# Kernel optimization log

Measured on AMD Instinct MI355X. Metric: run time of the kernel, lower is better.

Reference implementation:

```python
import jax, jax.numpy as jnp
import numpy as np

B, L, D, H = 4, 2048, 256, 8
FF = 128  # ff_intermediary_depth hard-coded in module
EPS = 1e-5


def layer_norm(x, g, b):
    mu = jnp.mean(x, axis=-1, keepdims=True)
    var = jnp.mean(jnp.square(x - mu), axis=-1, keepdims=True)
    return (x - mu) * jax.lax.rsqrt(var + EPS) * g + b


def setup_inputs() -> dict:
    key = jax.random.key(0)
    ks = jax.random.split(key, 8)
    s = 1.0 / np.sqrt(D)
    return {
        "seq": jax.random.normal(ks[0], (B, L, D), dtype=jnp.float32),
        "Wq": jax.random.normal(ks[1], (D, D * H), dtype=jnp.float32) * s,
        "Wk": jax.random.normal(ks[2], (D, D * H), dtype=jnp.float32) * s,
        "Wv": jax.random.normal(ks[3], (D, D * H), dtype=jnp.float32) * s,
        "Wo": jax.random.normal(ks[4], (D * H, D), dtype=jnp.float32) * (1.0 / np.sqrt(D * H)),
        "ln1_g": jnp.ones((D,), jnp.float32),
        "ln1_b": jnp.zeros((D,), jnp.float32),
        "W1": jax.random.normal(ks[5], (D, FF), dtype=jnp.float32) * s,
        "b1": jnp.zeros((FF,), jnp.float32),
        "W2": jax.random.normal(ks[6], (FF, D), dtype=jnp.float32) * (1.0 / np.sqrt(FF)),
        "b2": jnp.zeros((D,), jnp.float32),
        "ln2_g": jnp.ones((D,), jnp.float32),
        "ln2_b": jnp.zeros((D,), jnp.float32),
    }


def reference(seq, Wq, Wk, Wv, Wo, ln1_g, ln1_b, W1, b1, W2, b2, ln2_g, ln2_b):
    b, l, d = seq.shape
    # per-head dim equals full depth d (module quirk)
    q = (seq @ Wq).reshape(b, l, H, d)
    k = (seq @ Wk).reshape(b, l, H, d)
    v = (seq @ Wv).reshape(b, l, H, d)
    scores = jnp.einsum('bqhd,bkhd->bhqk', q, k) / jnp.sqrt(jnp.float32(d))
    a = jax.nn.softmax(scores, axis=-1)
    heads = jnp.einsum('bhqk,bkhd->bqhd', a, v).reshape(b, l, H * d)
    att_out = heads @ Wo
    x = layer_norm(seq + att_out, ln1_g, ln1_b)
    ff = jax.nn.relu(x @ W1 + b1) @ W2 + b2
    return layer_norm(x + ff, ln2_g, ln2_b)
```

## Files before the change

kernel.cpp:

```cpp
#include <hip/hip_runtime.h>


typedef unsigned short u16;
typedef unsigned int   u32;
typedef __bf16 bf16x8 __attribute__((ext_vector_type(8)));
typedef __bf16 bf16x2 __attribute__((ext_vector_type(2)));
typedef float  f32x4  __attribute__((ext_vector_type(4)));

#define MFMA(a, b, c) __builtin_amdgcn_mfma_f32_16x16x32_bf16(a, b, c, 0, 0, 0)

#if __has_builtin(__builtin_amdgcn_exp2f)
#define EXP2(x) __builtin_amdgcn_exp2f(x)
#else
#define EXP2(x) exp2f(x)
#endif

#if __has_builtin(__builtin_amdgcn_permlane16_swap) && \
    __has_builtin(__builtin_amdgcn_permlane32_swap)
#define HAS_PERMSWAP 1
#else
#define HAS_PERMSWAP 0
#endif

#define CEXP 0.09016844f

__device__ __forceinline__ float b2f(u16 h) {
  return __uint_as_float(((u32)h) << 16);
}
__device__ __forceinline__ u16 f2b(float f) {
  u32 u = __float_as_uint(f);
  u += 0x7FFFu + ((u >> 16) & 1u);
  return (u16)(u >> 16);
}
__device__ __forceinline__ u32 pkbf(float lo, float hi) {
  bf16x2 v;
  v[0] = (__bf16)lo;
  v[1] = (__bf16)hi;
  return __builtin_bit_cast(u32, v);
}
__device__ __forceinline__ bf16x8 ldb8(const u16* p) { return *(const bf16x8*)p; }

typedef const __attribute__((address_space(1))) u32* gas1_t;
typedef __attribute__((address_space(3))) u32* las3_t;
__device__ __forceinline__ void gload_lds16(const u16* g, u16* lds_base) {
  __builtin_amdgcn_global_load_lds((gas1_t)(const void*)g,
                                   (las3_t)(void*)lds_base, 16, 0, 0);
}

__device__ __forceinline__ int detect_f32(const void* seq) {
  const u32* s = (const u32*)seq;
  int cnt = 0;
  #pragma unroll
  for (int i = 0; i < 64; i++) {
    u32 e = (s[i] >> 7) & 0xFFu;
    cnt += (e >= 100u && e <= 140u) ? 1 : 0;
  }
  return cnt < 48;
}

__device__ __forceinline__ u16 ldw(const void* W, size_t idx, int isf32) {
  return isf32 ? f2b(((const float*)W)[idx]) : ((const u16*)W)[idx];
}

#if HAS_PERMSWAP
__device__ __forceinline__ bf16x8 softmax_pa(f32x4 sn0, f32x4 sn1,
                                             float& lsum) {
  float p00 = EXP2(sn0[0]), p01 = EXP2(sn0[1]);
  float p02 = EXP2(sn0[2]), p03 = EXP2(sn0[3]);
  float p10 = EXP2(sn1[0]), p11 = EXP2(sn1[1]);
  float p12 = EXP2(sn1[2]), p13 = EXP2(sn1[3]);
  lsum += ((p00 + p01) + (p02 + p03)) + ((p10 + p11) + (p12 + p13));
  u32 A0 = pkbf(p00, p01), A1 = pkbf(p02, p03);
  u32 B0 = pkbf(p10, p11), B1 = pkbf(p12, p13);
  auto ra = __builtin_amdgcn_permlane32_swap(A0, B0, false, false);
  auto rb = __builtin_amdgcn_permlane32_swap(A1, B1, false, false);
  auto sa = __builtin_amdgcn_permlane16_swap(ra[0], ra[1], false, false);
  auto sb = __builtin_amdgcn_permlane16_swap(rb[0], rb[1], false, false);
  uint4 wv;
  wv.x = sa[0];
  wv.y = sb[0];
  wv.z = sa[1];
  wv.w = sb[1];
  return __builtin_bit_cast(bf16x8, wv);
}
#endif

__global__ __launch_bounds__(256) void ingest_kernel(
    const void* __restrict__ seq, const void* __restrict__ g1,
    const void* __restrict__ be1, const void* __restrict__ b1,
    const void* __restrict__ b2v, const void* __restrict__ g2,
    const void* __restrict__ be2, u16* __restrict__ sbuf,
    u16* __restrict__ vecs) {
  int isf32 = detect_f32(seq);
  int bx = blockIdx.x, tid = threadIdx.x;
  if (bx < 2048) {
    size_t i = (size_t)bx * 1024 + tid * 4;
    if (isf32) {
      const float* sp = (const float*)seq;
      u16 o0 = f2b(sp[i]), o1 = f2b(sp[i + 1]), o2 = f2b(sp[i + 2]), o3 = f2b(sp[i + 3]);
      uint2 ov; ov.x = (u32)o0 | ((u32)o1 << 16); ov.y = (u32)o2 | ((u32)o3 << 16);
      *(uint2*)(sbuf + i) = ov;
    } else {
      *(uint2*)(sbuf + i) = ((const uint2*)seq)[i >> 2];
    }
  } else {
    int t = bx - 2048;
    const void* src; int n;
    switch (t) {
      case 0: src = g1;  n = 256; break;
      case 1: src = be1; n = 256; break;
      case 2: src = b1;  n = 128; break;
      case 3: src = b2v; n = 256; break;
      case 4: src = g2;  n = 256; break;
      default: src = be2; n = 256; break;
    }
    if (tid < n) vecs[t * 256 + tid] = ldw(src, tid, isf32);
  }
}

__global__ __launch_bounds__(256) void pack_kernel(
    const void* __restrict__ Wq, const void* __restrict__ Wk,
    const void* __restrict__ Wv, const void* __restrict__ Wo,
    const void* __restrict__ W1, const void* __restrict__ W2,
    const void* __restrict__ seq,
    u16* __restrict__ pWq, u16* __restrict__ pWk, u16* __restrict__ pWv,
    u16* __restrict__ pWo, u16* __restrict__ pW1, u16* __restrict__ pW2) {
  int isf32 = detect_f32(seq);
  const void* W; u16* P; int K, N;
  switch (blockIdx.y) {
    case 0: W = Wq; P = pWq; K = 256;  N = 2048; break;
    case 1: W = Wk; P = pWk; K = 256;  N = 2048; break;
    case 2: W = Wv; P = pWv; K = 256;  N = 2048; break;
    case 3: W = Wo; P = pWo; K = 2048; N = 256;  break;
    case 4: W = W1; P = pW1; K = 256;  N = 128;  break;
    default: W = W2; P = pW2; K = 128; N = 256;  break;
  }
  int t = blockIdx.x * 256 + threadIdx.x;
  int total = (K >> 5) * (N >> 4) * 64;
  if (t >= total) return;
  int lane = t & 63, f = t >> 6;
  int NT = N >> 4;
  int kt = f / NT, nt = f - kt * NT;
  int row0 = kt * 32 + ((lane >> 4) << 3);
  int col = nt * 16 + (lane & 15);
  u16 e[8];
  #pragma unroll
  for (int j = 0; j < 8; j++) e[j] = ldw(W, (size_t)(row0 + j) * N + col, isf32);
  uint4 u;
  u.x = (u32)e[0] | ((u32)e[1] << 16);
  u.y = (u32)e[2] | ((u32)e[3] << 16);
  u.z = (u32)e[4] | ((u32)e[5] << 16);
  u.w = (u32)e[6] | ((u32)e[7] << 16);
  *(uint4*)(P + ((size_t)f * 64 + lane) * 8) = u;
}

__global__ __launch_bounds__(256, 2) void qkv_kernel(
    const u16* __restrict__ X,
    const u16* __restrict__ pWq, const u16* __restrict__ pWk,
    const u16* __restrict__ pWv,
    u16* __restrict__ Qo, u16* __restrict__ Ko, u16* __restrict__ Vo,
    int ntbase, int hc) {
  __shared__ u16 blds[64 * 512];
  const u16* Pw = (blockIdx.z == 0) ? pWq : ((blockIdx.z == 1) ? pWk : pWv);
  u16* Out = (blockIdx.z == 0) ? Qo : ((blockIdx.z == 1) ? Ko : Vo);
  int tid = threadIdx.x, lane = tid & 63, w = tid >> 6;
  int nt0 = ntbase + blockIdx.x * 8;
  int m0 = blockIdx.y * 128 + w * 32;
  bf16x8 af[2][8];
  #pragma unroll
  for (int kt = 0; kt < 8; kt++) {
    af[0][kt] = ldb8(X + (size_t)(m0 + (lane & 15)) * 256 + kt * 32 + (lane >> 4) * 8);
    af[1][kt] = ldb8(X + (size_t)(m0 + 16 + (lane & 15)) * 256 + kt * 32 + (lane >> 4) * 8);
  }
  #pragma unroll
  for (int i = 0; i < 16; i++) {
    int fl = w + i * 4;
    int kt = fl >> 3, nt = fl & 7;
    gload_lds16(Pw + ((size_t)(kt * 128 + nt0 + nt) * 64 + lane) * 8,
                blds + (size_t)fl * 512);
  }
  asm volatile("s_waitcnt vmcnt(0)" ::: "memory");
  __syncthreads();
  f32x4 acc[2][8] = {};
  #pragma unroll
  for (int kt = 0; kt < 8; kt++) {
    const u16* bp = blds + (size_t)kt * 8 * 512 + (size_t)lane * 8;
    #pragma unroll
    for (int nt = 0; nt < 8; nt++) {
      bf16x8 b = ldb8(bp + nt * 512);
      acc[0][nt] = MFMA(af[0][kt], b, acc[0][nt]);
      acc[1][nt] = MFMA(af[1][kt], b, acc[1][nt]);
    }
  }
  int isv = (blockIdx.z == 2);
  float sc = (blockIdx.z == 0) ? CEXP : 1.0f;
  int hl = blockIdx.x >> 1;
  int dd0 = (blockIdx.x & 1) * 128;
  int m0b = blockIdx.y * 128;
  int bi = m0b >> 11, l0 = m0b & 2047;
  __syncthreads();
  if (!isv) {
    #pragma unroll
    for (int mt = 0; mt < 2; mt++)
      #pragma unroll
      for (int nt = 0; nt < 8; nt++)
        #pragma unroll
        for (int r = 0; r < 4; r++)
          blds[(w * 32 + mt * 16 + (lane >> 4) * 4 + r) * 136 + nt * 16 + (lane & 15)] =
              f2b(acc[mt][nt][r] * sc);
    __syncthreads();
    #pragma unroll
    for (int i = 0; i < 8; i++) {
      int c = tid + i * 256;
      int mloc = c >> 4, q = c & 15;
      uint4 v = *(uint4*)(blds + mloc * 136 + q * 8);
      *(uint4*)(Out + ((size_t)(bi * hc + hl) * 2048 + l0 + mloc) * 256 + dd0 + q * 8) = v;
    }
  } else {
    #pragma unroll
    for (int mt = 0; mt < 2; mt++)
      #pragma unroll
      for (int nt = 0; nt < 8; nt++)
        #pragma unroll
        for (int r = 0; r < 4; r++)
          blds[(nt * 16 + (lane & 15)) * 136 + w * 32 + mt * 16 + (lane >> 4) * 4 + r] =
              f2b(acc[mt][nt][r]);
    __syncthreads();
    #pragma unroll
    for (int i = 0; i < 8; i++) {
      int c = tid + i * 256;
      int nloc = c >> 4, q = c & 15;
      uint4 v = *(uint4*)(blds + nloc * 136 + q * 8);
      *(uint4*)(Out + ((size_t)(bi * hc + hl) * 256 + dd0 + nloc) * 2048 + l0 + q * 8) = v;
    }
  }
}

__global__ __launch_bounds__(512, 4) void attn_kernel(
    const u16* __restrict__ Q, const u16* __restrict__ K,
    const u16* __restrict__ Vt, u16* __restrict__ O, int nbh) {
  __shared__ u16 kbuf[2 * 8192];
  __shared__ u16 vbuf[2 * 8192];
#if !HAS_PERMSWAP
  __shared__ u16 plds[8 * 640];
#endif
  int tid = threadIdx.x, lane = tid & 63, w = tid >> 6;
  int bi2 = blockIdx.x;
  int bh, qt;
  if (nbh >= 8) {
    int G = nbh >> 3;
    bh = (bi2 & 7) * G + (bi2 >> 3) % G;
    qt = bi2 / (8 * G);
  } else {
    bh = bi2 % nbh; qt = bi2 / nbh;
  }
  const u16* Qb  = Q  + (size_t)bh * 2048 * 256;
  const u16* Kb  = K  + (size_t)bh * 2048 * 256;
  const u16* Vtb = Vt + (size_t)bh * 256 * 2048;
  u16* Ob = O + (size_t)bh * 2048 * 256;
  int q0 = qt * 128 + w * 16;
  bf16x8 qf[8];
  #pragma unroll
  for (int kt = 0; kt < 8; kt++)
    qf[kt] = ldb8(Qb + (size_t)(q0 + (lane & 15)) * 256 + kt * 32 + (lane >> 4) * 8);
  f32x4 o[16] = {};
  float lsum = 0.f;
#if !HAS_PERMSWAP
  u16* pl = plds + (size_t)w * 640;
#endif

  #pragma unroll
  for (int j = 0; j < 2; j++) {
    int f = w * 2 + j;
    gload_lds16(Kb + (size_t)((f >> 3) * 16 + (lane & 15)) * 256 +
                    (f & 7) * 32 + (lane >> 4) * 8,
                kbuf + f * 512);
    gload_lds16(Vtb + (size_t)(f * 16 + (lane & 15)) * 2048 + (lane >> 4) * 8,
                vbuf + f * 512);
  }

  for (int t = 0; t < 64; t++) {
    int s0i = t * 32;
    asm volatile("s_waitcnt vmcnt(0)\ns_barrier" ::: "memory");
    if (t < 63) {
      int nb = (t + 1) & 1;
      #pragma unroll
      for (int j = 0; j < 2; j++) {
        int f = w * 2 + j;
        gload_lds16(Kb + (size_t)(s0i + 32 + (f >> 3) * 16 + (lane & 15)) * 256 +
                        (f & 7) * 32 + (lane >> 4) * 8,
                    kbuf + nb * 8192 + f * 512);
        gload_lds16(Vtb + (size_t)(f * 16 + (lane & 15)) * 2048 + s0i + 32 +
                        (lane >> 4) * 8,
                    vbuf + nb * 8192 + f * 512);
      }
    }
    const u16* kb = kbuf + (t & 1) * 8192;
    f32x4 s[2] = {};
    __builtin_amdgcn_s_setprio(1);
    #pragma unroll
    for (int ntk = 0; ntk < 2; ntk++)
      #pragma unroll
      for (int kt = 0; kt < 8; kt++) {
        bf16x8 a = ldb8(kb + (size_t)(ntk * 8 + kt) * 512 + lane * 8);
        s[ntk] = MFMA(a, qf[kt], s[ntk]);
      }
    __builtin_amdgcn_s_setprio(0);
#if HAS_PERMSWAP
    bf16x8 pa = softmax_pa(s[0], s[1], lsum);
#else
    #pragma unroll
    for (int ntk = 0; ntk < 2; ntk++) {
      float p0 = EXP2(s[ntk][0]);
      float p1 = EXP2(s[ntk][1]);
      float p2 = EXP2(s[ntk][2]);
      float p3 = EXP2(s[ntk][3]);
      lsum += (p0 + p1) + (p2 + p3);
      uint2 pk;
      pk.x = pkbf(p0, p1);
      pk.y = pkbf(p2, p3);
      *(uint2*)(pl + (lane & 15) * 40 + 16 * ntk + 4 * (lane >> 4)) = pk;
    }
    asm volatile("s_waitcnt lgkmcnt(0)" ::: "memory");
    bf16x8 pa = ldb8(pl + (lane & 15) * 40 + (lane >> 4) * 8);
    asm volatile("s_waitcnt lgkmcnt(0)" ::: "memory");
#endif
    const u16* vb0 = vbuf + (t & 1) * 8192;
    __builtin_amdgcn_s_setprio(1);
    #pragma unroll
    for (int nt = 0; nt < 16; nt++) {
      bf16x8 vb = ldb8(vb0 + (size_t)nt * 512 + lane * 8);
      o[nt] = MFMA(vb, pa, o[nt]);
    }
    __builtin_amdgcn_s_setprio(0);
  }
  float l = lsum;
  l += __shfl_xor(l, 16);
  l += __shfl_xor(l, 32);
  float linv = 1.0f / l;
  u16* el = kbuf + w * 1152;
  __syncthreads();
  #pragma unroll
  for (int g = 0; g < 4; g++) {
    if (g) asm volatile("s_waitcnt lgkmcnt(0)" ::: "memory");
    #pragma unroll
    for (int t2 = 0; t2 < 4; t2++) {
      int nt = g * 4 + t2;
      uint2 pk;
      pk.x = pkbf(o[nt][0] * linv, o[nt][1] * linv);
      pk.y = pkbf(o[nt][2] * linv, o[nt][3] * linv);
      *(uint2*)(el + (lane & 15) * 72 + t2 * 16 + 4 * (lane >> 4)) = pk;
    }
    asm volatile("s_waitcnt lgkmcnt(0)" ::: "memory");
    #pragma unroll
    for (int rep = 0; rep < 2; rep++) {
      int ch = lane + rep * 64;
      int row = ch >> 3, c8 = ch & 7;
      uint4 v = *(uint4*)(el + row * 72 + c8 * 8);
      *(uint4*)(Ob + (size_t)(q0 + row) * 256 + g * 64 + c8 * 8) = v;
    }
  }
}

__global__ __launch_bounds__(128) void accum_ln1_kernel(
    const u16* __restrict__ Oc, const u16* __restrict__ pWo,
    const u16* __restrict__ sbuf, const u16* __restrict__ vecs,
    u16* __restrict__ xout) {
  __shared__ u16 blds[2 * 32 * 512];
  int tid = threadIdx.x, lane = tid & 63, w = tid >> 6;
  int m0 = blockIdx.x * 32 + w * 16;
  int arow = m0 + (lane & 15);
  int bq = arow >> 11, lrow = arow & 2047;
  f32x4 acc[16] = {};
  #pragma unroll
  for (int i = 0; i < 16; i++) {
    int fl = w + i * 2;
    int ktg = fl >> 4, nt = fl & 15;
    gload_lds16(pWo + ((size_t)(ktg * 16 + nt) * 64 + lane) * 8,
                blds + (size_t)fl * 512);
  }
  asm volatile("s_waitcnt vmcnt(0)" ::: "memory");
  __syncthreads();
  for (int r = 0; r < 32; r++) {
    int k0 = r * 2;
    const u16* cur = blds + (size_t)(r & 1) * 16384;
    bf16x8 aA, aB;
    {
      int ktl = k0, hl = ktl >> 3;
      int d0 = (ktl & 7) * 32 + (lane >> 4) * 8;
      aA = ldb8(Oc + ((size_t)(bq * 8 + hl) * 2048 + lrow) * 256 + d0);
      ktl = k0 + 1; hl = ktl >> 3;
      d0 = (ktl & 7) * 32 + (lane >> 4) * 8;
      aB = ldb8(Oc + ((size_t)(bq * 8 + hl) * 2048 + lrow) * 256 + d0);
    }
    if (r < 31) {
      u16* nxt = blds + (size_t)((r + 1) & 1) * 16384;
      #pragma unroll
      for (int i = 0; i < 16; i++) {
        int fl = w + i * 2;
        int ktg = k0 + 2 + (fl >> 4), nt = fl & 15;
        gload_lds16(pWo + ((size_t)(ktg * 16 + nt) * 64 + lane) * 8,
                    nxt + (size_t)fl * 512);
      }
    }
    #pragma unroll
    for (int kl = 0; kl < 2; kl++) {
      bf16x8 a = kl ? aB : aA;
      const u16* bp = cur + (size_t)kl * 16 * 512 + (size_t)lane * 8;
      #pragma unroll
      for (int nt = 0; nt < 16; nt++) {
        bf16x8 b = ldb8(bp + nt * 512);
        acc[nt] = MFMA(a, b, acc[nt]);
      }
    }
    asm volatile("s_waitcnt vmcnt(0)" ::: "memory");
    __syncthreads();
  }
  int rbase = m0 + (lane >> 4) * 4;
  #pragma unroll
  for (int nt = 0; nt < 16; nt++) {
    int d = nt * 16 + (lane & 15);
    #pragma unroll
    for (int r = 0; r < 4; r++)
      acc[nt][r] += b2f(sbuf[(size_t)(rbase + r) * 256 + d]);
  }
  float mu[4], rs[4];
  #pragma unroll
  for (int r = 0; r < 4; r++) {
    float sm = 0.f;
    #pragma unroll
    for (int nt = 0; nt < 16; nt++) sm += acc[nt][r];
    sm += __shfl_xor(sm, 1); sm += __shfl_xor(sm, 2);
    sm += __shfl_xor(sm, 4); sm += __shfl_xor(sm, 8);
    mu[r] = sm * (1.0f / 256.0f);
    float v = 0.f;
    #pragma unroll
    for (int nt = 0; nt < 16; nt++) { float dd = acc[nt][r] - mu[r]; v += dd * dd; }
    v += __shfl_xor(v, 1); v += __shfl_xor(v, 2);
    v += __shfl_xor(v, 4); v += __shfl_xor(v, 8);
    rs[r] = rsqrtf(v * (1.0f / 256.0f) + 1e-5f);
  }
  #pragma unroll
  for (int nt = 0; nt < 16; nt++) {
    int d = nt * 16 + (lane & 15);
    float gg = b2f(vecs[d]), bb = b2f(vecs[256 + d]);
    #pragma unroll
    for (int r = 0; r < 4; r++)
      xout[(size_t)(rbase + r) * 256 + d] = f2b((acc[nt][r] - mu[r]) * rs[r] * gg + bb);
  }
}

__global__ __launch_bounds__(256) void accum_kernel(
    const u16* __restrict__ Oc, const u16* __restrict__ pWo,
    float* __restrict__ att_out, int kt0, int hc) {
  __shared__ u16 blds[64 * 512];
  int tid = threadIdx.x, lane = tid & 63, w = tid >> 6;
  int m0 = blockIdx.x * 64 + w * 16;
  int arow = m0 + (lane & 15);
  int bq = arow >> 11, lrow = arow & 2047;
  int ktn = hc * 8;
  f32x4 acc[16] = {};
  for (int k0 = 0; k0 < ktn; k0 += 4) {
    __syncthreads();
    #pragma unroll
    for (int i = 0; i < 16; i++) {
      int fl = w + i * 4;
      int ktg = kt0 + k0 + (fl >> 4), nt = fl & 15;
      gload_lds16(pWo + ((size_t)(ktg * 16 + nt) * 64 + lane) * 8,
                  blds + (size_t)fl * 512);
    }
    asm volatile("s_waitcnt vmcnt(0)" ::: "memory");
    __syncthreads();
    #pragma unroll
    for (int kl = 0; kl < 4; kl++) {
      int ktl = k0 + kl;
      int hl = ktl >> 3;
      int d0 = (ktl & 7) * 32 + (lane >> 4) * 8;
      bf16x8 a = ldb8(Oc + ((size_t)(bq * hc + hl) * 2048 + lrow) * 256 + d0);
      const u16* bp = blds + (size_t)kl * 16 * 512 + (size_t)lane * 8;
      #pragma unroll
      for (int nt = 0; nt < 16; nt++) {
        bf16x8 b = ldb8(bp + nt * 512);
        acc[nt] = MFMA(a, b, acc[nt]);
      }
    }
  }
  int rbase = m0 + (lane >> 4) * 4;
  #pragma unroll
  for (int nt = 0; nt < 16; nt++) {
    int d = nt * 16 + (lane & 15);
    #pragma unroll
    for (int r = 0; r < 4; r++)
      att_out[(size_t)(rbase + r) * 256 + d] += acc[nt][r];
  }
}

__global__ __launch_bounds__(256) void ln1_kernel(
    const float* __restrict__ att_out, const u16* __restrict__ sbuf,
    const u16* __restrict__ vecs, u16* __restrict__ xout) {
  int tid = threadIdx.x, lane = tid & 63, w = tid >> 6;
  int row = blockIdx.x * 4 + w;
  const float* ar = att_out + (size_t)row * 256;
  f32x4 a = *(const f32x4*)(ar + lane * 4);
  uint2 sv = *(const uint2*)(sbuf + (size_t)row * 256 + lane * 4);
  float y[4];
  y[0] = a[0] + b2f((u16)(sv.x & 0xFFFF));
  y[1] = a[1] + b2f((u16)(sv.x >> 16));
  y[2] = a[2] + b2f((u16)(sv.y & 0xFFFF));
  y[3] = a[3] + b2f((u16)(sv.y >> 16));
  float sm = y[0] + y[1] + y[2] + y[3];
  sm += __shfl_xor(sm, 1);  sm += __shfl_xor(sm, 2);  sm += __shfl_xor(sm, 4);
  sm += __shfl_xor(sm, 8);  sm += __shfl_xor(sm, 16); sm += __shfl_xor(sm, 32);
  float mu = sm * (1.0f / 256.0f);
  float v = 0.f;
  #pragma unroll
  for (int j = 0; j < 4; j++) { float d = y[j] - mu; v += d * d; }
  v += __shfl_xor(v, 1);  v += __shfl_xor(v, 2);  v += __shfl_xor(v, 4);
  v += __shfl_xor(v, 8);  v += __shfl_xor(v, 16); v += __shfl_xor(v, 32);
  float rs = rsqrtf(v * (1.0f / 256.0f) + 1e-5f);
  u16 o[4];
  #pragma unroll
  for (int j = 0; j < 4; j++) {
    int d = lane * 4 + j;
    o[j] = f2b((y[j] - mu) * rs * b2f(vecs[d]) + b2f(vecs[256 + d]));
  }
  uint2 ov; ov.x = (u32)o[0] | ((u32)o[1] << 16); ov.y = (u32)o[2] | ((u32)o[3] << 16);
  *(uint2*)(xout + (size_t)row * 256 + lane * 4) = ov;
}

__global__ __launch_bounds__(128) void ffn_ln2_kernel(
    const u16* __restrict__ x, const u16* __restrict__ pW1,
    const u16* __restrict__ pW2, const u16* __restrict__ vecs,
    const void* __restrict__ seq, void* __restrict__ out) {
  __shared__ u16 hbuf[2 * 16 * 136];
  int isf32 = detect_f32(seq);
  int tid = threadIdx.x, lane = tid & 63, w = tid >> 6;
  int m0 = blockIdx.x * 32 + w * 16;
  int arow = m0 + (lane & 15);
  u16* hb = hbuf + w * 16 * 136;
  f32x4 acc1[8] = {};
  #pragma unroll
  for (int kt = 0; kt < 8; kt++) {
    bf16x8 a = ldb8(x + (size_t)arow * 256 + kt * 32 + (lane >> 4) * 8);
    const u16* bp = pW1 + ((size_t)kt * 8 * 64 + lane) * 8;
    #pragma unroll
    for (int nt = 0; nt < 8; nt++) {
      bf16x8 b = ldb8(bp + nt * 512);
      acc1[nt] = MFMA(a, b, acc1[nt]);
    }
  }
  #pragma unroll
  for (int nt = 0; nt < 8; nt++) {
    int col = nt * 16 + (lane & 15);
    float bb = b2f(vecs[512 + col]);
    #pragma unroll
    for (int r = 0; r < 4; r++) {
      float h = fmaxf(acc1[nt][r] + bb, 0.f);
      hb[((lane >> 4) * 4 + r) * 136 + col] = f2b(h);
    }
  }
  __syncthreads();
  f32x4 acc2[16] = {};
  #pragma unroll
  for (int ks = 0; ks < 4; ks++) {
    bf16x8 a = ldb8(hb + (lane & 15) * 136 + ks * 32 + (lane >> 4) * 8);
    const u16* bp = pW2 + ((size_t)ks * 16 * 64 + lane) * 8;
    #pragma unroll
    for (int nt = 0; nt < 16; nt++) {
      bf16x8 b = ldb8(bp + nt * 512);
      acc2[nt] = MFMA(a, b, acc2[nt]);
    }
  }
  int rbase = m0 + (lane >> 4) * 4;
  #pragma unroll
  for (int nt = 0; nt < 16; nt++) {
    int d = nt * 16 + (lane & 15);
    float bb = b2f(vecs[768 + d]);
    #pragma unroll
    for (int r = 0; r < 4; r++)
      acc2[nt][r] += bb + b2f(x[(size_t)(rbase + r) * 256 + d]);
  }
  float mu[4], rs[4];
  #pragma unroll
  for (int r = 0; r < 4; r++) {
    float sm = 0.f;
    #pragma unroll
    for (int nt = 0; nt < 16; nt++) sm += acc2[nt][r];
    sm += __shfl_xor(sm, 1); sm += __shfl_xor(sm, 2);
    sm += __shfl_xor(sm, 4); sm += __shfl_xor(sm, 8);
    mu[r] = sm * (1.0f / 256.0f);
    float v = 0.f;
    #pragma unroll
    for (int nt = 0; nt < 16; nt++) { float dd = acc2[nt][r] - mu[r]; v += dd * dd; }
    v += __shfl_xor(v, 1); v += __shfl_xor(v, 2);
    v += __shfl_xor(v, 4); v += __shfl_xor(v, 8);
    rs[r] = rsqrtf(v * (1.0f / 256.0f) + 1e-5f);
  }
  #pragma unroll
  for (int nt = 0; nt < 16; nt++) {
    int d = nt * 16 + (lane & 15);
    float gg = b2f(vecs[1024 + d]), bb = b2f(vecs[1280 + d]);
    #pragma unroll
    for (int r = 0; r < 4; r++) {
      float val = (acc2[nt][r] - mu[r]) * rs[r] * gg + bb;
      size_t idx = (size_t)(rbase + r) * 256 + d;
      if (isf32) ((float*)out)[idx] = val;
      else       ((u16*)out)[idx]   = f2b(val);
    }
  }
}

__global__ __launch_bounds__(256) void sentinel_kernel(void* out, int n,
                                                       const void* seq) {
  int isf32 = detect_f32(seq);
  int i = blockIdx.x * 256 + threadIdx.x;
  if (i < n) {
    if (isf32) ((float*)out)[i] = 777.0f;
    else       ((u16*)out)[i]   = 0x4442;
  }
}

extern "C" void kernel_launch(void* const* d_in, const int* in_sizes, int n_in,
                              void* d_out, int out_size, void* d_ws, size_t ws_size,
                              hipStream_t stream) {
  (void)in_sizes; (void)n_in;
  const void* seq  = d_in[0];
  const void* Wq   = d_in[1];
  const void* Wk   = d_in[2];
  const void* Wv   = d_in[3];
  const void* Wo   = d_in[4];
  const void* g1   = d_in[5];
  const void* be1  = d_in[6];
  const void* W1   = d_in[7];
  const void* b1   = d_in[8];
  const void* W2   = d_in[9];
  const void* b2   = d_in[10];
  const void* g2   = d_in[11];
  const void* be2  = d_in[12];

  size_t o = 0;
  u16* ws = (u16*)d_ws;
  u16* pWq = ws + o; o += 524288;
  u16* pWk = ws + o; o += 524288;
  u16* pWv = ws + o; o += 524288;
  u16* pWo = ws + o; o += 524288;
  u16* pW1 = ws + o; o += 32768;
  u16* pW2 = ws + o; o += 32768;
  float* att = (float*)(ws + o); o += 4194304;
  u16* xb   = ws + o; o += 2097152;
  u16* sbuf = ws + o; o += 2097152;
  u16* vecs = ws + o; o += 2048;
  size_t fixed_elems = o;

  int hc = 0;
  for (int c = 8; c >= 1; c >>= 1) {
    size_t need = (fixed_elems + (size_t)4 * c * 2097152) * 2;
    if (need <= ws_size) { hc = c; break; }
  }
  if (hc == 0) {
    sentinel_kernel<<<dim3((out_size + 255) / 256), 256, 0, stream>>>(
        d_out, out_size, seq);
    return;
  }
  u16* Qc = ws + o; o += (size_t)hc * 2097152;
  u16* Kc = ws + o; o += (size_t)hc * 2097152;
  u16* Vc = ws + o; o += (size_t)hc * 2097152;
  u16* Oc = ws + o;

  ingest_kernel<<<dim3(2054), 256, 0, stream>>>(seq, g1, be1, b1, b2, g2, be2,
                                                sbuf, vecs);
  pack_kernel<<<dim3(256, 6), 256, 0, stream>>>(Wq, Wk, Wv, Wo, W1, W2, seq,
                                                pWq, pWk, pWv, pWo, pW1, pW2);
  if (hc == 8) {
    qkv_kernel<<<dim3(16, 64, 3), 256, 0, stream>>>(
        sbuf, pWq, pWk, pWv, Qc, Kc, Vc, 0, 8);
    attn_kernel<<<dim3(32 * 16), 512, 0, stream>>>(Qc, Kc, Vc, Oc, 32);
    accum_ln1_kernel<<<dim3(256), 128, 0, stream>>>(Oc, pWo, sbuf, vecs, xb);
  } else {
    hipMemsetAsync(att, 0, 2097152 * sizeof(float), stream);
    int nchunks = 8 / hc;
    for (int c = 0; c < nchunks; c++) {
      int nbh = 4 * hc;
      qkv_kernel<<<dim3(2 * hc, 64, 3), 256, 0, stream>>>(
          sbuf, pWq, pWk, pWv, Qc, Kc, Vc, c * hc * 16, hc);
      attn_kernel<<<dim3(nbh * 16), 512, 0, stream>>>(Qc, Kc, Vc, Oc, nbh);
      accum_kernel<<<dim3(128), 256, 0, stream>>>(Oc, pWo, att, c * hc * 8, hc);
    }
    ln1_kernel<<<dim3(2048), 256, 0, stream>>>(att, sbuf, vecs, xb);
  }
  ffn_ln2_kernel<<<dim3(256), 128, 0, stream>>>(xb, pW1, pW2, vecs, seq,
                                                (void*)d_out);
}
```

Measured before the change: 342.3 us.

## Fuse ingest with weight packing and fold FFN+LN2 into accum_ln1

Merges the ingest and weight-pack kernels into one launch, and extends the attention-output accumulation + LN1 kernel to also run the FFN (W1, ReLU, W2) and LN2 on the same row tile, staging x and the hidden activations in LDS. This removes two kernel launches and the global round trip of the intermediate x buffer. In exchange the fused kernel has higher register pressure (extra accumulators and packed x kept in registers) and reads FFN weights straight from global memory per block.

Measured after the change: 341.8 us. Within noise of the previous version (-0.1%).

```diff
diff --git a/kernel.cpp b/kernel.cpp
--- a/kernel.cpp
+++ b/kernel.cpp
@@ -85,14 +85,13 @@
 }
 #endif
 
-__global__ __launch_bounds__(256) void ingest_kernel(
+__device__ __forceinline__ void ingest_body(
+    int bx, int tid, int isf32,
     const void* __restrict__ seq, const void* __restrict__ g1,
     const void* __restrict__ be1, const void* __restrict__ b1,
     const void* __restrict__ b2v, const void* __restrict__ g2,
     const void* __restrict__ be2, u16* __restrict__ sbuf,
     u16* __restrict__ vecs) {
-  int isf32 = detect_f32(seq);
-  int bx = blockIdx.x, tid = threadIdx.x;
   if (bx < 2048) {
     size_t i = (size_t)bx * 1024 + tid * 4;
     if (isf32) {
@@ -118,16 +117,15 @@
   }
 }
 
-__global__ __launch_bounds__(256) void pack_kernel(
+__device__ __forceinline__ void pack_body(
+    int px, int py, int tid, int isf32,
     const void* __restrict__ Wq, const void* __restrict__ Wk,
     const void* __restrict__ Wv, const void* __restrict__ Wo,
     const void* __restrict__ W1, const void* __restrict__ W2,
-    const void* __restrict__ seq,
     u16* __restrict__ pWq, u16* __restrict__ pWk, u16* __restrict__ pWv,
     u16* __restrict__ pWo, u16* __restrict__ pW1, u16* __restrict__ pW2) {
-  int isf32 = detect_f32(seq);
   const void* W; u16* P; int K, N;
-  switch (blockIdx.y) {
+  switch (py) {
     case 0: W = Wq; P = pWq; K = 256;  N = 2048; break;
     case 1: W = Wk; P = pWk; K = 256;  N = 2048; break;
     case 2: W = Wv; P = pWv; K = 256;  N = 2048; break;
@@ -135,7 +133,7 @@
     case 4: W = W1; P = pW1; K = 256;  N = 128;  break;
     default: W = W2; P = pW2; K = 128; N = 256;  break;
   }
-  int t = blockIdx.x * 256 + threadIdx.x;
+  int t = px * 256 + tid;
   int total = (K >> 5) * (N >> 4) * 64;
   if (t >= total) return;
   int lane = t & 63, f = t >> 6;
@@ -152,6 +150,28 @@
   u.z = (u32)e[4] | ((u32)e[5] << 16);
   u.w = (u32)e[6] | ((u32)e[7] << 16);
   *(uint4*)(P + ((size_t)f * 64 + lane) * 8) = u;
+}
+
+__global__ __launch_bounds__(256) void ingest_pack_kernel(
+    const void* __restrict__ seq, const void* __restrict__ g1,
+    const void* __restrict__ be1, const void* __restrict__ b1,
+    const void* __restrict__ b2v, const void* __restrict__ g2,
+    const void* __restrict__ be2, u16* __restrict__ sbuf,
+    u16* __restrict__ vecs,
+    const void* __restrict__ Wq, const void* __restrict__ Wk,
+    const void* __restrict__ Wv, const void* __restrict__ Wo,
+    const void* __restrict__ W1, const void* __restrict__ W2,
+    u16* __restrict__ pWq, u16* __restrict__ pWk, u16* __restrict__ pWv,
+    u16* __restrict__ pWo, u16* __restrict__ pW1, u16* __restrict__ pW2) {
+  int isf32 = detect_f32(seq);
+  int bx = blockIdx.x, tid = threadIdx.x;
+  if (bx < 2054) {
+    ingest_body(bx, tid, isf32, seq, g1, be1, b1, b2v, g2, be2, sbuf, vecs);
+  } else {
+    int bxp = bx - 2054;
+    pack_body(bxp & 255, bxp >> 8, tid, isf32, Wq, Wk, Wv, Wo, W1, W2,
+              pWq, pWk, pWv, pWo, pW1, pW2);
+  }
 }
 
 __global__ __launch_bounds__(256, 2) void qkv_kernel(
@@ -362,10 +382,11 @@
   }
 }
 
-__global__ __launch_bounds__(128) void accum_ln1_kernel(
+__global__ __launch_bounds__(128) void accum_ln1_ffn_ln2_kernel(
     const u16* __restrict__ Oc, const u16* __restrict__ pWo,
     const u16* __restrict__ sbuf, const u16* __restrict__ vecs,
-    u16* __restrict__ xout) {
+    const u16* __restrict__ pW1, const u16* __restrict__ pW2,
+    const void* __restrict__ seq, void* __restrict__ out) {
   __shared__ u16 blds[2 * 32 * 512];
   int tid = threadIdx.x, lane = tid & 63, w = tid >> 6;
   int m0 = blockIdx.x * 32 + w * 16;
@@ -440,13 +461,93 @@
     v += __shfl_xor(v, 4); v += __shfl_xor(v, 8);
     rs[r] = rsqrtf(v * (1.0f / 256.0f) + 1e-5f);
   }
+  u16* xw = blds + (size_t)w * 16 * 264;
+  uint2 xp[16];
   #pragma unroll
   for (int nt = 0; nt < 16; nt++) {
     int d = nt * 16 + (lane & 15);
     float gg = b2f(vecs[d]), bb = b2f(vecs[256 + d]);
-    #pragma unroll
-    for (int r = 0; r < 4; r++)
-      xout[(size_t)(rbase + r) * 256 + d] = f2b((acc[nt][r] - mu[r]) * rs[r] * gg + bb);
+    u16 e[4];
+    #pragma unroll
+    for (int r = 0; r < 4; r++) {
+      e[r] = f2b((acc[nt][r] - mu[r]) * rs[r] * gg + bb);
+      xw[((lane >> 4) * 4 + r) * 264 + d] = e[r];
+    }
+    xp[nt].x = (u32)e[0] | ((u32)e[1] << 16);
+    xp[nt].y = (u32)e[2] | ((u32)e[3] << 16);
+  }
+  __syncthreads();
+  int isf32 = detect_f32(seq);
+  u16* hb = blds + 16384 + (size_t)w * 16 * 136;
+  f32x4 acc1[8] = {};
+  #pragma unroll
+  for (int kt = 0; kt < 8; kt++) {
+    bf16x8 a = ldb8(xw + (size_t)(lane & 15) * 264 + kt * 32 + (lane >> 4) * 8);
+    const u16* bp = pW1 + ((size_t)kt * 8 * 64 + lane) * 8;
+    #pragma unroll
+    for (int nt = 0; nt < 8; nt++) {
+      bf16x8 b = ldb8(bp + nt * 512);
+      acc1[nt] = MFMA(a, b, acc1[nt]);
+    }
+  }
+  #pragma unroll
+  for (int nt = 0; nt < 8; nt++) {
+    int col = nt * 16 + (lane & 15);
+    float bb = b2f(vecs[512 + col]);
+    #pragma unroll
+    for (int r = 0; r < 4; r++) {
+      float h = fmaxf(acc1[nt][r] + bb, 0.f);
+      hb[((lane >> 4) * 4 + r) * 136 + col] = f2b(h);
+    }
+  }
+  __syncthreads();
+  f32x4 acc2[16] = {};
+  #pragma unroll
+  for (int ks = 0; ks < 4; ks++) {
+    bf16x8 a = ldb8(hb + (size_t)(lane & 15) * 136 + ks * 32 + (lane >> 4) * 8);
+    const u16* bp = pW2 + ((size_t)ks * 16 * 64 + lane) * 8;
+    #pragma unroll
+    for (int nt = 0; nt < 16; nt++) {
+      bf16x8 b = ldb8(bp + nt * 512);
+      acc2[nt] = MFMA(a, b, acc2[nt]);
+    }
+  }
+  #pragma unroll
+  for (int nt = 0; nt < 16; nt++) {
+    int d = nt * 16 + (lane & 15);
+    float bb = b2f(vecs[768 + d]);
+    acc2[nt][0] += bb + b2f((u16)(xp[nt].x & 0xFFFF));
+    acc2[nt][1] += bb + b2f((u16)(xp[nt].x >> 16));
+    acc2[nt][2] += bb + b2f((u16)(xp[nt].y & 0xFFFF));
+    acc2[nt][3] += bb + b2f((u16)(xp[nt].y >> 16));
+  }
+  float mu2[4], rs2[4];
+  #pragma unroll
+  for (int r = 0; r < 4; r++) {
+    float sm = 0.f;
+    #pragma unroll
+    for (int nt = 0; nt < 16; nt++) sm += acc2[nt][r];
+    sm += __shfl_xor(sm, 1); sm += __shfl_xor(sm, 2);
+    sm += __shfl_xor(sm, 4); sm += __shfl_xor(sm, 8);
+    mu2[r] = sm * (1.0f / 256.0f);
+    float v = 0.f;
+    #pragma unroll
+    for (int nt = 0; nt < 16; nt++) { float dd = acc2[nt][r] - mu2[r]; v += dd * dd; }
+    v += __shfl_xor(v, 1); v += __shfl_xor(v, 2);
+    v += __shfl_xor(v, 4); v += __shfl_xor(v, 8);
+    rs2[r] = rsqrtf(v * (1.0f / 256.0f) + 1e-5f);
+  }
+  #pragma unroll
+  for (int nt = 0; nt < 16; nt++) {
+    int d = nt * 16 + (lane & 15);
+    float gg = b2f(vecs[1024 + d]), bb = b2f(vecs[1280 + d]);
+    #pragma unroll
+    for (int r = 0; r < 4; r++) {
+      float val = (acc2[nt][r] - mu2[r]) * rs2[r] * gg + bb;
+      size_t idx = (size_t)(rbase + r) * 256 + d;
+      if (isf32) ((float*)out)[idx] = val;
+      else       ((u16*)out)[idx]   = f2b(val);
+    }
   }
 }
 
@@ -667,15 +768,15 @@
   u16* Vc = ws + o; o += (size_t)hc * 2097152;
   u16* Oc = ws + o;
 
-  ingest_kernel<<<dim3(2054), 256, 0, stream>>>(seq, g1, be1, b1, b2, g2, be2,
-                                                sbuf, vecs);
-  pack_kernel<<<dim3(256, 6), 256, 0, stream>>>(Wq, Wk, Wv, Wo, W1, W2, seq,
-                                                pWq, pWk, pWv, pWo, pW1, pW2);
+  ingest_pack_kernel<<<dim3(2054 + 1536), 256, 0, stream>>>(
+      seq, g1, be1, b1, b2, g2, be2, sbuf, vecs,
+      Wq, Wk, Wv, Wo, W1, W2, pWq, pWk, pWv, pWo, pW1, pW2);
   if (hc == 8) {
     qkv_kernel<<<dim3(16, 64, 3), 256, 0, stream>>>(
         sbuf, pWq, pWk, pWv, Qc, Kc, Vc, 0, 8);
     attn_kernel<<<dim3(32 * 16), 512, 0, stream>>>(Qc, Kc, Vc, Oc, 32);
-    accum_ln1_kernel<<<dim3(256), 128, 0, stream>>>(Oc, pWo, sbuf, vecs, xb);
+    accum_ln1_ffn_ln2_kernel<<<dim3(256), 128, 0, stream>>>(
+        Oc, pWo, sbuf, vecs, pW1, pW2, seq, (void*)d_out);
   } else {
     hipMemsetAsync(att, 0, 2097152 * sizeof(float), stream);
     int nchunks = 8 / hc;
@@ -687,7 +788,7 @@
       accum_kernel<<<dim3(128), 256, 0, stream>>>(Oc, pWo, att, c * hc * 8, hc);
     }
     ln1_kernel<<<dim3(2048), 256, 0, stream>>>(att, sbuf, vecs, xb);
-  }
-  ffn_ln2_kernel<<<dim3(256), 128, 0, stream>>>(xb, pW1, pW2, vecs, seq,
-                                                (void*)d_out);
-}
+    ffn_ln2_kernel<<<dim3(256), 128, 0, stream>>>(xb, pW1, pW2, vecs, seq,
+                                                  (void*)d_out);
+  }
+}
```
